# Kernel tuning notes

Measured on AMD Instinct MI355X. Metric: run time of the kernel, lower is better.

Reference implementation:

```python
import math
import jax, jax.numpy as jnp
import numpy as np

B, S, E, H, DK, NW = 2048, 1, 1024, 128, 8, 8  # d_k == n_wires == 8, seq_len must be 1
DIM = 2 ** NW


def setup_inputs() -> dict:
    key = jax.random.key(0)
    ks = jax.random.split(key, 7)
    scale = 1.0 / math.sqrt(E)
    return {
        "x": jax.random.normal(ks[0], (B, S, E), jnp.float32),
        "wq": jax.random.normal(ks[1], (E, E), jnp.float32) * scale,
        "wk": jax.random.normal(ks[2], (E, E), jnp.float32) * scale,
        "wv": jax.random.normal(ks[3], (E, E), jnp.float32) * scale,
        "wc": jax.random.normal(ks[4], (E, E), jnp.float32) * scale,
        "bc": jax.random.normal(ks[5], (E,), jnp.float32) * 0.01,
        "rx_params": jax.random.normal(ks[6], (NW,), jnp.float32),  # trainable RX angles (shared q_layer)
    }


def _apply_rx(state, theta, wire):
    # state: (N, 2,...,2) [NW qubit axes]; theta: scalar or (N,)
    N = state.shape[0]
    theta = jnp.broadcast_to(theta, (N,))
    c = jnp.cos(theta * 0.5).astype(jnp.complex64)[:, None]
    s = (-1j * jnp.sin(theta * 0.5).astype(jnp.complex64))[:, None]
    st = jnp.moveaxis(state, wire + 1, 1).reshape(N, 2, -1)
    new = jnp.stack([c * st[:, 0] + s * st[:, 1],
                     s * st[:, 0] + c * st[:, 1]], axis=1)
    return jnp.moveaxis(new.reshape((N,) + (2,) * NW), 1, wire + 1)


def _apply_cnot(state, ctrl, tgt):
    st = jnp.moveaxis(state, (ctrl + 1, tgt + 1), (1, 2))
    st = jnp.stack([st[:, 0], jnp.flip(st[:, 1], axis=1)], axis=1)
    return jnp.moveaxis(st, (1, 2), (ctrl + 1, tgt + 1))


def _qlayer(angles, rx_params):
    # angles: (N, NW) per-sample RX encoder angles; rx_params: (NW,) shared trainable RX
    N = angles.shape[0]
    state = jnp.zeros((N,) + (2,) * NW, jnp.complex64)
    state = state.at[(slice(None),) + (0,) * NW].set(1.0 + 0j)  # |0...0>
    for w in range(NW):
        state = _apply_rx(state, angles[:, w], w)      # encoder RX(x_w)
    for w in range(NW):
        state = _apply_rx(state, rx_params[w], w)      # trainable RX
    for w in range(NW - 1):
        state = _apply_cnot(state, w, w + 1)           # CNOT chain
    state = _apply_cnot(state, NW - 1, 0)              # ring closure
    probs = jnp.abs(state.reshape(N, DIM)) ** 2
    bits = (jnp.arange(DIM)[:, None] >> jnp.arange(NW - 1, -1, -1)[None, :]) & 1  # wire 0 = MSB
    signs = (1.0 - 2.0 * bits).astype(jnp.float32)     # (DIM, NW)
    return probs @ signs                               # <Z_w> per wire, (N, NW)


def reference(x, wq, wk, wv, wc, bc, rx_params):
    q = jnp.einsum('bse,fe->bsf', x, wq).reshape(B, S, H, DK)
    k = jnp.einsum('bse,fe->bsf', x, wk).reshape(B, S, H, DK)
    v = jnp.einsum('bse,fe->bsf', x, wv).reshape(B, S, H, DK)
    scores = jnp.einsum('bqhd,bkhd->bhqk', q, k) / math.sqrt(DK)
    attn = jax.nn.softmax(scores, axis=-1)             # dropout is identity in eval
    out = jnp.einsum('bhqk,bkhd->bqhd', attn, v).reshape(B, S, E)
    # per-head quantum circuit (S==1, d_k==NW); batch all heads together
    angles = out.reshape(B * H, DK)
    qout = _qlayer(angles, rx_params).reshape(B, S, E)
    return jnp.einsum('bse,fe->bsf', qout, wc) + bc
```

## Files before the change

### kernel.cpp

```cpp
#include <hip/hip_runtime.h>
#include <hip/hip_bf16.h>
#include <math.h>


#define BB 2048
#define EN 1024
#define LDA 40

typedef short s16x8 __attribute__((ext_vector_type(8)));
typedef float f32x4 __attribute__((ext_vector_type(4)));

union Frag { s16x8 v; __hip_bfloat16 h[8]; };

__device__ inline s16x8 cvt_frag(f32x4 lo, f32x4 hi) {
    Frag u;
    #pragma unroll
    for (int j = 0; j < 4; ++j) {
        u.h[j]     = __float2bfloat16(lo[j]);
        u.h[4 + j] = __float2bfloat16(hi[j]);
    }
    return u.v;
}

__global__ __launch_bounds__(256) void cvt3_kernel(
        const float* __restrict__ x, const float* __restrict__ wv,
        const float* __restrict__ wc,
        __hip_bfloat16* __restrict__ xb, __hip_bfloat16* __restrict__ wvb,
        __hip_bfloat16* __restrict__ wcb, int nx)
{
    const int g = blockIdx.x * 256 + threadIdx.x;
    const int NG = (EN * EN) / 8;
    const float* s; __hip_bfloat16* d; size_t off;
    if (g < nx)           { s = x;  d = xb;  off = (size_t)g * 8; }
    else if (g < nx + NG) { s = wv; d = wvb; off = (size_t)(g - nx) * 8; }
    else                  { s = wc; d = wcb; off = (size_t)(g - nx - NG) * 8; }
    f32x4 lo = *(const f32x4*)(s + off);
    f32x4 hi = *(const f32x4*)(s + off + 4);
    *(s16x8*)(d + off) = cvt_frag(lo, hi);
}

template <bool AF32, int EPI>
__global__ __launch_bounds__(256, 4) void gemm_kernel(
        const void* __restrict__ Av, const __hip_bfloat16* __restrict__ Wb,
        const float* __restrict__ bias, void* __restrict__ Cv)
{
    __shared__ __hip_bfloat16 As[128 * LDA];
    __shared__ __hip_bfloat16 Bs[64 * LDA];

    const int tid  = threadIdx.x;
    const int wave = tid >> 6, lane = tid & 63;
    const int l15 = lane & 15, lq = lane >> 4;
    const int m0 = blockIdx.x * 128, n0 = blockIdx.y * 64;
    const int wm = (wave & 1) * 64, wn = (wave >> 1) * 32;

    const int sr = tid >> 2;
    const int sk = (tid & 3) * 8;
    const float*          af = (const float*)Av;
    const __hip_bfloat16* ab = (const __hip_bfloat16*)Av;
    __hip_bfloat16* aw0 = &As[sr * LDA + sk];
    __hip_bfloat16* aw1 = &As[(sr + 64) * LDA + sk];
    __hip_bfloat16* bw  = &Bs[sr * LDA + sk];

    auto g_load = [&](int kk, s16x8& ra0, s16x8& ra1, s16x8& rb) {
        if (AF32) {
            const float* p0 = af + (size_t)(m0 + sr) * EN + kk + sk;
            const float* p1 = p0 + (size_t)64 * EN;
            ra0 = cvt_frag(*(const f32x4*)p0, *(const f32x4*)(p0 + 4));
            ra1 = cvt_frag(*(const f32x4*)p1, *(const f32x4*)(p1 + 4));
        } else {
            const __hip_bfloat16* p0 = ab + (size_t)(m0 + sr) * EN + kk + sk;
            ra0 = *(const s16x8*)p0;
            ra1 = *(const s16x8*)(p0 + (size_t)64 * EN);
        }
        rb = *(const s16x8*)(Wb + (size_t)(n0 + sr) * EN + kk + sk);
    };

    f32x4 acc[4][2] = {};

    s16x8 ra0, ra1, rb;
    g_load(0, ra0, ra1, rb);
    *(s16x8*)aw0 = ra0; *(s16x8*)aw1 = ra1; *(s16x8*)bw = rb;
    __syncthreads();

    for (int kk = 32; kk <= EN; kk += 32) {
        const bool more = (kk < EN);
        s16x8 na0, na1, nb;
        if (more) g_load(kk, na0, na1, nb);

        s16x8 a[4], b[2];
        #pragma unroll
        for (int i = 0; i < 4; ++i)
            a[i] = *(const s16x8*)&As[(wm + 16 * i + l15) * LDA + lq * 8];
        #pragma unroll
        for (int j = 0; j < 2; ++j)
            b[j] = *(const s16x8*)&Bs[(wn + 16 * j + l15) * LDA + lq * 8];
        #pragma unroll
        for (int i = 0; i < 4; ++i)
            #pragma unroll
            for (int j = 0; j < 2; ++j)
                acc[i][j] = __builtin_amdgcn_mfma_f32_16x16x32_bf16(
                                a[i], b[j], acc[i][j], 0, 0, 0);

        __syncthreads();
        if (more) {
            *(s16x8*)aw0 = na0; *(s16x8*)aw1 = na1; *(s16x8*)bw = nb;
        }
        __syncthreads();
    }

    if (EPI == 0) {
        __hip_bfloat16* C = (__hip_bfloat16*)Cv;
        #pragma unroll
        for (int i = 0; i < 4; ++i)
            #pragma unroll
            for (int j = 0; j < 2; ++j) {
                const int col = n0 + wn + 16 * j + l15;
                #pragma unroll
                for (int r = 0; r < 4; ++r) {
                    const int row = m0 + wm + 16 * i + lq * 4 + r;
                    C[(size_t)row * EN + col] = __float2bfloat16(acc[i][j][r]);
                }
            }
    } else {
        float* C = (float*)Cv;
        #pragma unroll
        for (int j = 0; j < 2; ++j) {
            const int col = n0 + wn + 16 * j + l15;
            const float bv = bias[col];
            #pragma unroll
            for (int i = 0; i < 4; ++i)
                #pragma unroll
                for (int r = 0; r < 4; ++r) {
                    const int row = m0 + wm + 16 * i + lq * 4 + r;
                    C[(size_t)row * EN + col] = acc[i][j][r] + bv;
                }
        }
    }
}

__global__ __launch_bounds__(256) void quantum_kernel(
        __hip_bfloat16* __restrict__ V, const float* __restrict__ rx)
{
    const int g = blockIdx.x * 256 + threadIdx.x;
    Frag in;
    in.v = *(const s16x8*)(V + (size_t)g * 8);
    float t[8];
    #pragma unroll
    for (int j = 0; j < 8; ++j)
        t[j] = cosf(__bfloat162float(in.h[j]) + rx[j]);

    Frag o;
    float suf = t[1];
    #pragma unroll
    for (int j = 2; j < 8; ++j) suf *= t[j];
    o.h[0] = __float2bfloat16(suf);
    float p = t[0];
    #pragma unroll
    for (int j = 1; j < 8; ++j) { p *= t[j]; o.h[j] = __float2bfloat16(p); }

    *(s16x8*)(V + (size_t)g * 8) = o.v;
}

extern "C" void kernel_launch(void* const* d_in, const int* in_sizes, int n_in,
                              void* d_out, int out_size, void* d_ws, size_t ws_size,
                              hipStream_t stream)
{
    const float* x  = (const float*)d_in[0];
    const float* wv = (const float*)d_in[3];
    const float* wc = (const float*)d_in[4];
    const float* bc = (const float*)d_in[5];
    const float* rx = (const float*)d_in[6];
    float* out = (float*)d_out;

    const size_t XE = (size_t)BB * EN;
    const size_t WE = (size_t)EN * EN;
    dim3 grid(BB / 128, EN / 64);

    if (ws_size >= (XE + 2 * WE + XE) * sizeof(__hip_bfloat16)) {
        __hip_bfloat16* xb  = (__hip_bfloat16*)d_ws;
        __hip_bfloat16* wvb = xb + XE;
        __hip_bfloat16* wcb = wvb + WE;
        __hip_bfloat16* V   = wcb + WE;
        cvt3_kernel<<<(int)((XE / 8 + 2 * (WE / 8)) / 256), 256, 0, stream>>>(
            x, wv, wc, xb, wvb, wcb, (int)(XE / 8));
        gemm_kernel<false, 0><<<grid, 256, 0, stream>>>(xb, wvb, nullptr, V);
        quantum_kernel<<<(int)(XE / 8 / 256), 256, 0, stream>>>(V, rx);
        gemm_kernel<false, 1><<<grid, 256, 0, stream>>>(V, wcb, bc, out);
    } else {
        __hip_bfloat16* wvb = (__hip_bfloat16*)d_ws;
        __hip_bfloat16* wcb = wvb + WE;
        __hip_bfloat16* V   = wcb + WE;
        cvt3_kernel<<<(int)(2 * (WE / 8) / 256), 256, 0, stream>>>(
            x, wv, wc, nullptr, wvb, wcb, 0);
        gemm_kernel<true, 0><<<grid, 256, 0, stream>>>(x, wvb, nullptr, V);
        quantum_kernel<<<(int)(XE / 8 / 256), 256, 0, stream>>>(V, rx);
        gemm_kernel<false, 1><<<grid, 256, 0, stream>>>(V, wcb, bc, out);
    }
}
```

Baseline: 115.5 us.

## Stage GEMM tiles with direct global-to-LDS loads and double buffering

Rewrites the bf16 GEMM so it uses global_load_lds to copy 16-byte chunks straight into LDS in MFMA fragment order. LDS is double buffered with a 64-wide K step, and the block tile shrinks to 64x64, which doubles the grid. The aim is to remove the register round trip and one barrier per K step, and to overlap loads with MFMA work. The workspace-size fallback is also dropped, so the code now assumes the workspace is large enough, and smaller tiles mean less reuse per block.

After: 116.2 us. About the same (+0.6%).

```diff
diff --git a/kernel.cpp b/kernel.cpp
--- a/kernel.cpp
+++ b/kernel.cpp
@@ -5,7 +5,6 @@
 
 #define BB 2048
 #define EN 1024
-#define LDA 40
 
 typedef short s16x8 __attribute__((ext_vector_type(8)));
 typedef float f32x4 __attribute__((ext_vector_type(4)));
@@ -20,6 +19,13 @@
         u.h[4 + j] = __float2bfloat16(hi[j]);
     }
     return u.v;
+}
+
+__device__ inline void gll16(const __hip_bfloat16* g, __hip_bfloat16* l) {
+    __builtin_amdgcn_global_load_lds(
+        (const __attribute__((address_space(1))) void*)g,
+        (__attribute__((address_space(3))) void*)l,
+        16, 0, 0);
 }
 
 __global__ __launch_bounds__(256) void cvt3_kernel(
@@ -39,100 +45,95 @@
     *(s16x8*)(d + off) = cvt_frag(lo, hi);
 }
 
-template <bool AF32, int EPI>
-__global__ __launch_bounds__(256, 4) void gemm_kernel(
-        const void* __restrict__ Av, const __hip_bfloat16* __restrict__ Wb,
-        const float* __restrict__ bias, void* __restrict__ Cv)
+template <int EPI>
+__global__ __launch_bounds__(256, 2) void gemm_kernel(
+        const __hip_bfloat16* __restrict__ A,
+        const __hip_bfloat16* __restrict__ W,
+        const float* __restrict__ bias,
+        void* __restrict__ Cv)
 {
-    __shared__ __hip_bfloat16 As[128 * LDA];
-    __shared__ __hip_bfloat16 Bs[64 * LDA];
+    __shared__ __hip_bfloat16 lds[16384];
 
     const int tid  = threadIdx.x;
     const int wave = tid >> 6, lane = tid & 63;
     const int l15 = lane & 15, lq = lane >> 4;
-    const int m0 = blockIdx.x * 128, n0 = blockIdx.y * 64;
-    const int wm = (wave & 1) * 64, wn = (wave >> 1) * 32;
+    const int m0 = blockIdx.x * 64, n0 = blockIdx.y * 64;
+    const int wm = (wave & 1) * 32, wn = (wave >> 1) * 32;
 
-    const int sr = tid >> 2;
-    const int sk = (tid & 3) * 8;
-    const float*          af = (const float*)Av;
-    const __hip_bfloat16* ab = (const __hip_bfloat16*)Av;
-    __hip_bfloat16* aw0 = &As[sr * LDA + sk];
-    __hip_bfloat16* aw1 = &As[(sr + 64) * LDA + sk];
-    __hip_bfloat16* bw  = &Bs[sr * LDA + sk];
+    const __hip_bfloat16* gsrc[4];
+    int ldst[4];
+    #pragma unroll
+    for (int i = 0; i < 4; ++i) {
+        const int t  = wave * 4 + i;
+        const int kt = t & 1;
+        int row, lofs;
+        const __hip_bfloat16* base;
+        if (t < 8) { const int mt = t >> 1;       row = m0 + mt * 16 + l15; base = A; lofs = t * 512; }
+        else       { const int nt = (t - 8) >> 1; row = n0 + nt * 16 + l15; base = W; lofs = 4096 + (t - 8) * 512; }
+        gsrc[i] = base + (size_t)row * EN + kt * 32 + lq * 8;
+        ldst[i] = lofs;
+    }
 
-    auto g_load = [&](int kk, s16x8& ra0, s16x8& ra1, s16x8& rb) {
-        if (AF32) {
-            const float* p0 = af + (size_t)(m0 + sr) * EN + kk + sk;
-            const float* p1 = p0 + (size_t)64 * EN;
-            ra0 = cvt_frag(*(const f32x4*)p0, *(const f32x4*)(p0 + 4));
-            ra1 = cvt_frag(*(const f32x4*)p1, *(const f32x4*)(p1 + 4));
-        } else {
-            const __hip_bfloat16* p0 = ab + (size_t)(m0 + sr) * EN + kk + sk;
-            ra0 = *(const s16x8*)p0;
-            ra1 = *(const s16x8*)(p0 + (size_t)64 * EN);
-        }
-        rb = *(const s16x8*)(Wb + (size_t)(n0 + sr) * EN + kk + sk);
-    };
+    f32x4 acc[2][2] = {};
 
-    f32x4 acc[4][2] = {};
-
-    s16x8 ra0, ra1, rb;
-    g_load(0, ra0, ra1, rb);
-    *(s16x8*)aw0 = ra0; *(s16x8*)aw1 = ra1; *(s16x8*)bw = rb;
+    #pragma unroll
+    for (int i = 0; i < 4; ++i) gll16(gsrc[i], &lds[ldst[i]]);
     __syncthreads();
 
-    for (int kk = 32; kk <= EN; kk += 32) {
-        const bool more = (kk < EN);
-        s16x8 na0, na1, nb;
-        if (more) g_load(kk, na0, na1, nb);
-
-        s16x8 a[4], b[2];
+    int p = 0;
+    for (int k0 = 64; k0 <= EN; k0 += 64) {
+        if (k0 < EN) {
+            const int q = p ^ 1;
+            #pragma unroll
+            for (int i = 0; i < 4; ++i) gll16(gsrc[i] + k0, &lds[q * 8192 + ldst[i]]);
+        }
+        const __hip_bfloat16* Ab = &lds[p * 8192];
+        const __hip_bfloat16* Bb = Ab + 4096;
         #pragma unroll
-        for (int i = 0; i < 4; ++i)
-            a[i] = *(const s16x8*)&As[(wm + 16 * i + l15) * LDA + lq * 8];
-        #pragma unroll
-        for (int j = 0; j < 2; ++j)
-            b[j] = *(const s16x8*)&Bs[(wn + 16 * j + l15) * LDA + lq * 8];
-        #pragma unroll
-        for (int i = 0; i < 4; ++i)
+        for (int kt = 0; kt < 2; ++kt) {
+            s16x8 a[2], b[2];
             #pragma unroll
-            for (int j = 0; j < 2; ++j)
-                acc[i][j] = __builtin_amdgcn_mfma_f32_16x16x32_bf16(
-                                a[i], b[j], acc[i][j], 0, 0, 0);
-
-        __syncthreads();
-        if (more) {
-            *(s16x8*)aw0 = na0; *(s16x8*)aw1 = na1; *(s16x8*)bw = nb;
+            for (int mi = 0; mi < 2; ++mi)
+                a[mi] = *(const s16x8*)&Ab[((wm >> 4) + mi) * 1024 + kt * 512 + lane * 8];
+            #pragma unroll
+            for (int nj = 0; nj < 2; ++nj)
+                b[nj] = *(const s16x8*)&Bb[((wn >> 4) + nj) * 1024 + kt * 512 + lane * 8];
+            #pragma unroll
+            for (int mi = 0; mi < 2; ++mi)
+                #pragma unroll
+                for (int nj = 0; nj < 2; ++nj)
+                    acc[mi][nj] = __builtin_amdgcn_mfma_f32_16x16x32_bf16(
+                                      a[mi], b[nj], acc[mi][nj], 0, 0, 0);
         }
         __syncthreads();
+        p ^= 1;
     }
 
     if (EPI == 0) {
         __hip_bfloat16* C = (__hip_bfloat16*)Cv;
         #pragma unroll
-        for (int i = 0; i < 4; ++i)
+        for (int mi = 0; mi < 2; ++mi)
             #pragma unroll
-            for (int j = 0; j < 2; ++j) {
-                const int col = n0 + wn + 16 * j + l15;
+            for (int nj = 0; nj < 2; ++nj) {
+                const int col = n0 + wn + nj * 16 + l15;
                 #pragma unroll
                 for (int r = 0; r < 4; ++r) {
-                    const int row = m0 + wm + 16 * i + lq * 4 + r;
-                    C[(size_t)row * EN + col] = __float2bfloat16(acc[i][j][r]);
+                    const int row = m0 + wm + mi * 16 + lq * 4 + r;
+                    C[(size_t)row * EN + col] = __float2bfloat16(acc[mi][nj][r]);
                 }
             }
     } else {
         float* C = (float*)Cv;
         #pragma unroll
-        for (int j = 0; j < 2; ++j) {
-            const int col = n0 + wn + 16 * j + l15;
+        for (int nj = 0; nj < 2; ++nj) {
+            const int col = n0 + wn + nj * 16 + l15;
             const float bv = bias[col];
             #pragma unroll
-            for (int i = 0; i < 4; ++i)
+            for (int mi = 0; mi < 2; ++mi)
                 #pragma unroll
                 for (int r = 0; r < 4; ++r) {
-                    const int row = m0 + wm + 16 * i + lq * 4 + r;
-                    C[(size_t)row * EN + col] = acc[i][j][r] + bv;
+                    const int row = m0 + wm + mi * 16 + lq * 4 + r;
+                    C[(size_t)row * EN + col] = acc[mi][nj][r] + bv;
                 }
         }
     }
@@ -174,26 +175,16 @@
 
     const size_t XE = (size_t)BB * EN;
     const size_t WE = (size_t)EN * EN;
-    dim3 grid(BB / 128, EN / 64);
 
-    if (ws_size >= (XE + 2 * WE + XE) * sizeof(__hip_bfloat16)) {
-        __hip_bfloat16* xb  = (__hip_bfloat16*)d_ws;
-        __hip_bfloat16* wvb = xb + XE;
-        __hip_bfloat16* wcb = wvb + WE;
-        __hip_bfloat16* V   = wcb + WE;
-        cvt3_kernel<<<(int)((XE / 8 + 2 * (WE / 8)) / 256), 256, 0, stream>>>(
-            x, wv, wc, xb, wvb, wcb, (int)(XE / 8));
-        gemm_kernel<false, 0><<<grid, 256, 0, stream>>>(xb, wvb, nullptr, V);
-        quantum_kernel<<<(int)(XE / 8 / 256), 256, 0, stream>>>(V, rx);
-        gemm_kernel<false, 1><<<grid, 256, 0, stream>>>(V, wcb, bc, out);
-    } else {
-        __hip_bfloat16* wvb = (__hip_bfloat16*)d_ws;
-        __hip_bfloat16* wcb = wvb + WE;
-        __hip_bfloat16* V   = wcb + WE;
-        cvt3_kernel<<<(int)(2 * (WE / 8) / 256), 256, 0, stream>>>(
-            x, wv, wc, nullptr, wvb, wcb, 0);
-        gemm_kernel<true, 0><<<grid, 256, 0, stream>>>(x, wvb, nullptr, V);
-        quantum_kernel<<<(int)(XE / 8 / 256), 256, 0, stream>>>(V, rx);
-        gemm_kernel<false, 1><<<grid, 256, 0, stream>>>(V, wcb, bc, out);
-    }
+    __hip_bfloat16* xb  = (__hip_bfloat16*)d_ws;
+    __hip_bfloat16* wvb = xb + XE;
+    __hip_bfloat16* wcb = wvb + WE;
+    __hip_bfloat16* V   = wcb + WE;
+
+    dim3 grid(BB / 64, EN / 64);
+    cvt3_kernel<<<(int)((XE / 8 + 2 * (WE / 8)) / 256), 256, 0, stream>>>(
+        x, wv, wc, xb, wvb, wcb, (int)(XE / 8));
+    gemm_kernel<0><<<grid, 256, 0, stream>>>(xb, wvb, nullptr, V);
+    quantum_kernel<<<(int)(XE / 8 / 256), 256, 0, stream>>>(V, rx);
+    gemm_kernel<1><<<grid, 256, 0, stream>>>(V, wcb, bc, out);
 }
```
